# Kernel optimization log

Hardware: AMD Instinct MI355X
Metric: run time of the kernel (lower is better)

Reference implementation:

```python
import jax, jax.numpy as jnp
import numpy as np

SIGMA = 0.5
BETA = 0.3
NEG_MODES = 2
EPS = 1e-12


def _l2norm(v, axis):
    n = jnp.sqrt(jnp.sum(v * v, axis=axis, keepdims=True))
    return v / jnp.maximum(n, EPS)


def setup_inputs() -> dict:
    key = jax.random.key(0)
    ks = jax.random.split(key, 6)
    B, Cin, H, W = 16, 256, 64, 64
    E, R = 256, 365
    x = jax.random.normal(ks[0], (B, Cin, H, W), dtype=jnp.float32)
    conv_w = jax.random.normal(ks[1], (E, Cin), dtype=jnp.float32) * 0.02
    conv_b = jax.random.normal(ks[2], (E,), dtype=jnp.float32) * 0.02
    reps = jax.random.normal(ks[3], (R, 1, E), dtype=jnp.float32)
    # stored representations were L2-normalized over the channel dim during training
    representations = _l2norm(reps, axis=2)
    neg_w = jax.random.normal(ks[4], (E * NEG_MODES, E), dtype=jnp.float32) * 0.01
    neg_b = jax.random.normal(ks[5], (E * NEG_MODES,), dtype=jnp.float32) * 0.01
    return {"x": x, "conv_w": conv_w, "conv_b": conv_b,
            "representations": representations, "neg_w": neg_w, "neg_b": neg_b}


def _distance(reps, emb):
    # reps: [R, M, E], emb: [B, E, H, W] (both unit-normalized)
    # ||e - r||^2 = ||e||^2 + ||r||^2 - 2 e.r  -- avoids the 6D broadcast tensor
    dot = jnp.einsum('behw,rme->brmhw', emb, reps)
    en2 = jnp.sum(emb * emb, axis=1)          # [B, H, W]
    rn2 = jnp.sum(reps * reps, axis=2)        # [R, M]
    d2 = en2[:, None, None] + rn2[None, :, :, None, None] - 2.0 * dot
    return jnp.sqrt(jnp.maximum(d2, 0.0))


def reference(x, conv_w, conv_b, representations, neg_w, neg_b):
    # emb_module: 1x1 conv, then L2-normalize over channels (dim=1)
    emb = jnp.einsum('bchw,ec->behw', x, conv_w) + conv_b[None, :, None, None]
    emb = _l2norm(emb, axis=1)

    reps = jax.lax.stop_gradient(representations)        # [R, 1, E] (detached)
    R, _, E = reps.shape
    neg_offset = (jnp.abs(reps[:, 0, :]) @ neg_w.T + neg_b).reshape(R, NEG_MODES, E)
    reps_neg = (neg_offset + jnp.abs(reps)) * jnp.sign(reps)   # broadcast [R,1,E]->[R,2,E]
    reps_neg = _l2norm(reps_neg, axis=2)

    distance = _distance(reps, emb)          # [B, R, 1, H, W]
    distance_neg = _distance(reps_neg, emb)  # [B, R, 2, H, W]

    inv2s2 = 1.0 / (2.0 * SIGMA ** 2)
    probs_neg = jnp.exp(-(distance_neg ** 2) * inv2s2)
    cls_score_neg = jnp.max(probs_neg, axis=2)               # [B, R, H, W]
    probs_ori = jnp.max(jnp.exp(-(distance ** 2) * inv2s2), axis=2)

    dn_min = jnp.min(distance_neg, axis=2, keepdims=True)    # [B, R, 1, H, W]
    probs = jnp.exp(-((distance + BETA * (2.0 - dn_min)) ** 2) * inv2s2)

    # cls_norm=True branch
    probs_sumj = jnp.sum(probs, axis=2)                      # [B, R, H, W]
    probs_sumij = jnp.sum(probs_sumj, axis=1, keepdims=True)
    cls_score = probs_sumj / probs_sumij

    return (cls_score, cls_score_neg, distance, distance_neg, probs_ori)
```

## Files before the change

### kernel.cpp

```cpp
#include <hip/hip_runtime.h>

#define BATCH   16
#define CIN     256
#define EDIM    256
#define HW      4096
#define NPIX    65536
#define RREAL   365
#define RPAD    368
#define NCHUNK  23
#define OUTPLANE 23920640
#define ESTRIDE 264

typedef __attribute__((ext_vector_type(8))) short short8;
typedef __attribute__((ext_vector_type(4))) float f32x4;

__device__ __forceinline__ unsigned short f2bf(float f) {
    union { float f; unsigned u; } v; v.f = f;
    unsigned r = v.u + 0x7fffu + ((v.u >> 16) & 1u);
    return (unsigned short)(r >> 16);
}

__global__ __launch_bounds__(256) void k_reps(const float* __restrict__ reps,
                                              const float* __restrict__ negw,
                                              const float* __restrict__ negb,
                                              const float* __restrict__ convw,
                                              unsigned short* __restrict__ wbf,
                                              unsigned short* __restrict__ rp,
                                              unsigned short* __restrict__ rn0,
                                              unsigned short* __restrict__ rn1) {
    int r = blockIdx.x;
    int t = threadIdx.x;
    if (r < 256) wbf[r*256 + t] = f2bf(convw[r*256 + t]);
    if (r >= RREAL) {
        rp[r*256 + t] = 0; rn0[r*256 + t] = 0; rn1[r*256 + t] = 0;
        return;
    }
    __shared__ __align__(16) float sa[256];
    __shared__ float outo[512];
    __shared__ float red[8];
    float rv = reps[r*256 + t];
    float av = fabsf(rv);
    sa[t] = av;
    __syncthreads();
    int wid = t >> 6, lane = t & 63;
    const f32x4* a4 = (const f32x4*)sa;
    f32x4 a = a4[lane];
    #pragma unroll 4
    for (int i = 0; i < 128; i++) {
        int e = wid*128 + i;
        f32x4 wv = *(const f32x4*)(negw + (size_t)e*256 + lane*4);
        float p = wv[0]*a[0] + wv[1]*a[1] + wv[2]*a[2] + wv[3]*a[3];
        #pragma unroll
        for (int off = 32; off; off >>= 1) p += __shfl_xor(p, off);
        if (lane == 0) outo[e] = p + negb[e];
    }
    __syncthreads();
    float sgn = (rv > 0.f) ? 1.f : ((rv < 0.f) ? -1.f : 0.f);
    float v0 = (outo[t] + av) * sgn;
    float v1 = (outo[256 + t] + av) * sgn;
    float s0 = v0*v0, s1 = v1*v1;
    #pragma unroll
    for (int off = 32; off; off >>= 1) { s0 += __shfl_xor(s0, off); s1 += __shfl_xor(s1, off); }
    if ((t & 63) == 0) { red[wid] = s0; red[4 + wid] = s1; }
    __syncthreads();
    float t0 = red[0] + red[1] + red[2] + red[3];
    float t1 = red[4] + red[5] + red[6] + red[7];
    float i0 = 1.f / fmaxf(sqrtf(t0), 1e-12f);
    float i1 = 1.f / fmaxf(sqrtf(t1), 1e-12f);
    rp [r*256 + t] = f2bf(rv);
    rn0[r*256 + t] = f2bf(v0 * i0);
    rn1[r*256 + t] = f2bf(v1 * i1);
}

__global__ __launch_bounds__(256) void k_fused(const float* __restrict__ x,
                                               const unsigned short* __restrict__ wbf,
                                               const float* __restrict__ convb,
                                               const unsigned short* __restrict__ rp,
                                               const unsigned short* __restrict__ rn0,
                                               const unsigned short* __restrict__ rn1,
                                               float* __restrict__ oCls,
                                               float* __restrict__ oClsNeg,
                                               float* __restrict__ oDist,
                                               float* __restrict__ oDneg,
                                               float* __restrict__ oPori,
                                               float* __restrict__ sumij) {
    __shared__ unsigned short elds[4][16][ESTRIDE];
    int wave = threadIdx.x >> 6, lane = threadIdx.x & 63;
    int l15 = lane & 15, quad = lane >> 4;
    int px0 = blockIdx.x * 64 + wave * 16;
    int b = px0 >> 12, hw0 = px0 & 4095;
    const float* xb = x + (size_t)b * CIN * HW;
    int hwa = hw0 + l15;

    f32x4 acc[16];
    #pragma unroll
    for (int et = 0; et < 16; et++) acc[et] = (f32x4){0.f, 0.f, 0.f, 0.f};
    for (int k0 = 0; k0 < 8; k0++) {
        int c0 = k0 * 32 + quad * 8;
        short8 af;
        #pragma unroll
        for (int j = 0; j < 8; j++) {
            float xv = xb[(size_t)(c0 + j) * HW + hwa];
            ((unsigned short*)&af)[j] = f2bf(xv);
        }
        #pragma unroll
        for (int et = 0; et < 16; et++) {
            short8 bf = *(const short8*)(wbf + (size_t)(et*16 + l15) * 256 + k0*32 + quad*8);
            acc[et] = __builtin_amdgcn_mfma_f32_16x16x32_bf16(af, bf, acc[et], 0, 0, 0);
        }
    }
    float cb[16];
    #pragma unroll
    for (int et = 0; et < 16; et++) cb[et] = convb[et*16 + l15];
    #pragma unroll
    for (int reg = 0; reg < 4; reg++) {
        int pl = quad * 4 + reg;
        float v[16]; float s = 0.f;
        #pragma unroll
        for (int et = 0; et < 16; et++) {
            float vv = acc[et][reg] + cb[et];
            v[et] = vv; s += vv * vv;
        }
        s += __shfl_xor(s, 1); s += __shfl_xor(s, 2);
        s += __shfl_xor(s, 4); s += __shfl_xor(s, 8);
        float inv = 1.f / fmaxf(sqrtf(s), 1e-12f);
        #pragma unroll
        for (int et = 0; et < 16; et++)
            elds[wave][pl][et*16 + l15] = f2bf(v[et] * inv);
    }
    __syncthreads();

    short8 ef[8];
    #pragma unroll
    for (int k0 = 0; k0 < 8; k0++)
        ef[k0] = *(const short8*)&elds[wave][l15][k0*32 + quad*8];

    size_t obase = (size_t)b * RREAL * HW;
    int hwq = hw0 + quad * 4;
    size_t rowb = obase        + ((size_t)l15 << 12) + hwq;
    size_t idnb = (obase << 1) + ((size_t)l15 << 13) + hwq;
    f32x4 sumP = (f32x4){0.f, 0.f, 0.f, 0.f};

    for (int ch = 0; ch < NCHUNK; ch++) {
        int r = ch * 16 + l15;
        size_t rrow = (size_t)r * 256 + quad * 8;
        f32x4 aP  = (f32x4){0.f,0.f,0.f,0.f};
        f32x4 aN0 = (f32x4){0.f,0.f,0.f,0.f};
        f32x4 aN1 = (f32x4){0.f,0.f,0.f,0.f};
        #pragma unroll
        for (int k0 = 0; k0 < 8; k0++) {
            short8 fp = *(const short8*)(rp  + rrow + k0*32);
            short8 f0 = *(const short8*)(rn0 + rrow + k0*32);
            short8 f1 = *(const short8*)(rn1 + rrow + k0*32);
            aP  = __builtin_amdgcn_mfma_f32_16x16x32_bf16(ef[k0], fp, aP , 0, 0, 0);
            aN0 = __builtin_amdgcn_mfma_f32_16x16x32_bf16(ef[k0], f0, aN0, 0, 0, 0);
            aN1 = __builtin_amdgcn_mfma_f32_16x16x32_bf16(ef[k0], f1, aN1, 0, 0, 0);
        }
        f32x4 vD, vPori, vCneg, vCls, vDn0, vDn1;
        #pragma unroll
        for (int c = 0; c < 4; c++) {
            float d2 = fmaxf(2.f - 2.f * aP [c], 0.f);
            float e0 = fmaxf(2.f - 2.f * aN0[c], 0.f);
            float e1 = fmaxf(2.f - 2.f * aN1[c], 0.f);
            float d   = sqrtf(d2);
            float dn0 = sqrtf(e0);
            float dn1 = sqrtf(e1);
            vD[c]    = d;
            vDn0[c]  = dn0;
            vDn1[c]  = dn1;
            vPori[c] = __expf(-2.f * d2);
            float pn0 = __expf(-2.f * e0);
            float pn1 = __expf(-2.f * e1);
            vCneg[c] = fmaxf(pn0, pn1);
            float dnmin = fminf(dn0, dn1);
            float tt = fmaf(-0.3f, dnmin, d + 0.6f);
            vCls[c]  = __expf(-2.f * tt * tt);
        }
        if (r < RREAL) {
            size_t row = rowb + ((size_t)ch << 16);
            *(f32x4*)(oDist   + row) = vD;
            *(f32x4*)(oPori   + row) = vPori;
            *(f32x4*)(oClsNeg + row) = vCneg;
            *(f32x4*)(oCls    + row) = vCls;
            size_t idn = idnb + ((size_t)ch << 17);
            *(f32x4*)(oDneg + idn)      = vDn0;
            *(f32x4*)(oDneg + idn + HW) = vDn1;
            sumP += vCls;
        }
    }
    #pragma unroll
    for (int off = 1; off <= 8; off <<= 1) {
        sumP[0] += __shfl_xor(sumP[0], off);
        sumP[1] += __shfl_xor(sumP[1], off);
        sumP[2] += __shfl_xor(sumP[2], off);
        sumP[3] += __shfl_xor(sumP[3], off);
    }
    if (l15 == 0)
        *(f32x4*)(sumij + px0 + quad * 4) = sumP;
}

__global__ __launch_bounds__(256) void k_div(float* __restrict__ oCls,
                                             const float* __restrict__ sumij) {
    int bb = blockIdx.y;
    size_t off = (size_t)blockIdx.x * 1024 + threadIdx.x * 4;
    int hw = (int)(off & 4095);
    float* p = oCls + (size_t)bb * ((size_t)RREAL * HW) + off;
    f32x4 v = *(f32x4*)p;
    f32x4 s = *(const f32x4*)(sumij + bb * HW + hw);
    v[0] /= s[0]; v[1] /= s[1]; v[2] /= s[2]; v[3] /= s[3];
    *(f32x4*)p = v;
}

extern "C" void kernel_launch(void* const* d_in, const int* in_sizes, int n_in,
                              void* d_out, int out_size, void* d_ws, size_t ws_size,
                              hipStream_t stream) {
    const float* x      = (const float*)d_in[0];
    const float* conv_w = (const float*)d_in[1];
    const float* conv_b = (const float*)d_in[2];
    const float* reps   = (const float*)d_in[3];
    const float* neg_w  = (const float*)d_in[4];
    const float* neg_b  = (const float*)d_in[5];
    float* out = (float*)d_out;

    char* ws = (char*)d_ws;
    unsigned short* rp  = (unsigned short*)ws;
    unsigned short* rn0 = rp  + RPAD * 256;
    unsigned short* rn1 = rn0 + RPAD * 256;
    unsigned short* wbf = rn1 + RPAD * 256;
    float* sumij = (float*)(ws + 3 * RPAD * 256 * 2 + 65536 * 2);

    float* oCls    = out;
    float* oClsNeg = out + (size_t)OUTPLANE;
    float* oDist   = out + (size_t)OUTPLANE * 2;
    float* oDneg   = out + (size_t)OUTPLANE * 3;
    float* oPori   = out + (size_t)OUTPLANE * 5;

    k_reps <<<RPAD, 256, 0, stream>>>(reps, neg_w, neg_b, conv_w, wbf, rp, rn0, rn1);
    k_fused<<<NPIX / 64, 256, 0, stream>>>(x, wbf, conv_b, rp, rn0, rn1,
                                           oCls, oClsNeg, oDist, oDneg, oPori, sumij);
    k_div  <<<dim3(RREAL * HW / 1024, BATCH), 256, 0, stream>>>(oCls, sumij);
}
```

Measured before the change: 953.6 us.

## Shrink fused blocks to two waves, halve LDS staging, swizzle tile order, use rcp

The fused kernel now runs 128-thread blocks covering 32 pixels instead of 256 threads covering 64. The embedding transpose through LDS is done in two halves with a half-size buffer, and the separate value array is dropped by writing back into the accumulators. Block indices are remapped so consecutive blocks are spread across eight pixel regions, and the division pass uses a hardware reciprocal instead of true division. The aim is higher occupancy and lower LDS and register pressure, at the cost of extra barriers and slightly less precise normalisation.

```diff
diff --git a/kernel.cpp b/kernel.cpp
--- a/kernel.cpp
+++ b/kernel.cpp
@@ -9,7 +9,7 @@
 #define RPAD    368
 #define NCHUNK  23
 #define OUTPLANE 23920640
-#define ESTRIDE 264
+#define ESH     136
 
 typedef __attribute__((ext_vector_type(8))) short short8;
 typedef __attribute__((ext_vector_type(4))) float f32x4;
@@ -72,7 +72,7 @@
     rn1[r*256 + t] = f2bf(v1 * i1);
 }
 
-__global__ __launch_bounds__(256) void k_fused(const float* __restrict__ x,
+__global__ __launch_bounds__(128) void k_fused(const float* __restrict__ x,
                                                const unsigned short* __restrict__ wbf,
                                                const float* __restrict__ convb,
                                                const unsigned short* __restrict__ rp,
@@ -84,10 +84,11 @@
                                                float* __restrict__ oDneg,
                                                float* __restrict__ oPori,
                                                float* __restrict__ sumij) {
-    __shared__ unsigned short elds[4][16][ESTRIDE];
+    __shared__ unsigned short elds[2][16][ESH];
     int wave = threadIdx.x >> 6, lane = threadIdx.x & 63;
     int l15 = lane & 15, quad = lane >> 4;
-    int px0 = blockIdx.x * 64 + wave * 16;
+    int tile = (blockIdx.x & 7) * 256 + (blockIdx.x >> 3);
+    int px0 = tile * 32 + wave * 16;
     int b = px0 >> 12, hw0 = px0 & 4095;
     const float* xb = x + (size_t)b * CIN * HW;
     int hwa = hw0 + l15;
@@ -112,28 +113,35 @@
     float cb[16];
     #pragma unroll
     for (int et = 0; et < 16; et++) cb[et] = convb[et*16 + l15];
+    float inv[4];
     #pragma unroll
     for (int reg = 0; reg < 4; reg++) {
-        int pl = quad * 4 + reg;
-        float v[16]; float s = 0.f;
+        float s = 0.f;
         #pragma unroll
         for (int et = 0; et < 16; et++) {
             float vv = acc[et][reg] + cb[et];
-            v[et] = vv; s += vv * vv;
+            acc[et][reg] = vv; s += vv * vv;
         }
         s += __shfl_xor(s, 1); s += __shfl_xor(s, 2);
         s += __shfl_xor(s, 4); s += __shfl_xor(s, 8);
-        float inv = 1.f / fmaxf(sqrtf(s), 1e-12f);
-        #pragma unroll
-        for (int et = 0; et < 16; et++)
-            elds[wave][pl][et*16 + l15] = f2bf(v[et] * inv);
-    }
-    __syncthreads();
-
+        inv[reg] = 1.f / fmaxf(sqrtf(s), 1e-12f);
+    }
     short8 ef[8];
     #pragma unroll
-    for (int k0 = 0; k0 < 8; k0++)
-        ef[k0] = *(const short8*)&elds[wave][l15][k0*32 + quad*8];
+    for (int h = 0; h < 2; h++) {
+        #pragma unroll
+        for (int reg = 0; reg < 4; reg++) {
+            int pl = quad * 4 + reg;
+            #pragma unroll
+            for (int et = h*8; et < h*8 + 8; et++)
+                elds[wave][pl][(et - h*8)*16 + l15] = f2bf(acc[et][reg] * inv[reg]);
+        }
+        __syncthreads();
+        #pragma unroll
+        for (int k = 0; k < 4; k++)
+            ef[h*4 + k] = *(const short8*)&elds[wave][l15][k*32 + quad*8];
+        __syncthreads();
+    }
 
     size_t obase = (size_t)b * RREAL * HW;
     int hwq = hw0 + quad * 4;
@@ -207,7 +215,10 @@
     float* p = oCls + (size_t)bb * ((size_t)RREAL * HW) + off;
     f32x4 v = *(f32x4*)p;
     f32x4 s = *(const f32x4*)(sumij + bb * HW + hw);
-    v[0] /= s[0]; v[1] /= s[1]; v[2] /= s[2]; v[3] /= s[3];
+    v[0] *= __builtin_amdgcn_rcpf(s[0]);
+    v[1] *= __builtin_amdgcn_rcpf(s[1]);
+    v[2] *= __builtin_amdgcn_rcpf(s[2]);
+    v[3] *= __builtin_amdgcn_rcpf(s[3]);
     *(f32x4*)p = v;
 }
 
@@ -236,7 +247,7 @@
     float* oPori   = out + (size_t)OUTPLANE * 5;
 
     k_reps <<<RPAD, 256, 0, stream>>>(reps, neg_w, neg_b, conv_w, wbf, rp, rn0, rn1);
-    k_fused<<<NPIX / 64, 256, 0, stream>>>(x, wbf, conv_b, rp, rn0, rn1,
+    k_fused<<<NPIX / 32, 128, 0, stream>>>(x, wbf, conv_b, rp, rn0, rn1,
                                            oCls, oClsNeg, oDist, oDneg, oPori, sumij);
     k_div  <<<dim3(RREAL * HW / 1024, BATCH), 256, 0, stream>>>(oCls, sumij);
 }
```

After: 999.1 us. 1.05x slower.
